# Kernel tuning notes

Hardware: AMD Instinct MI355X
Metric: run time of the kernel (lower is better)

The kernel has to match this reference:

```python
import jax, jax.numpy as jnp
import numpy as np

EPS = 1e-12  # torch F.normalize eps

def _l2norm(v, axis):
    n = jnp.sqrt(jnp.sum(v * v, axis=axis, keepdims=True))
    return v / jnp.maximum(n, EPS)

def setup_inputs() -> dict:
    key = jax.random.key(0)
    k1, k2, k3 = jax.random.split(key, 3)
    N, D, H, W, K = 32, 512, 56, 56, 64
    x = jax.random.normal(k1, (N, D, H, W), dtype=jnp.float32)
    conv_w = jax.random.normal(k2, (K, D), dtype=jnp.float32) * 0.05
    centroids = jax.random.uniform(k3, (K, D), dtype=jnp.float32)
    return {"x": x, "conv_w": conv_w, "centroids": centroids}

def reference(x, conv_w, centroids):
    N, D, H, W = x.shape
    K = centroids.shape[0]
    # descriptor-wise L2 normalization over channel dim
    x = _l2norm(x, axis=1)
    x_flat = x.reshape(N, D, H * W)                      # (N, D, P)
    # 1x1 conv == per-pixel linear map: (K,D) x (N,D,P) -> (N,K,P)
    logits = jnp.einsum('kd,ndp->nkp', conv_w, x_flat)
    soft_assign = jax.nn.softmax(logits, axis=1)         # softmax over clusters
    # vlad[n,k,:] = sum_p a[n,k,p] * (x[n,:,p] - c[k,:])
    #            = (a @ x^T)[n,k,:] - (sum_p a[n,k,p]) * c[k,:]
    agg = jnp.einsum('nkp,ndp->nkd', soft_assign, x_flat)           # (N, K, D)
    a_sum = jnp.sum(soft_assign, axis=2)                            # (N, K)
    vlad = agg - a_sum[:, :, None] * centroids[None, :, :]
    vlad = _l2norm(vlad, axis=2)        # intra-normalization per cluster
    vlad = vlad.reshape(N, K * D)
    vlad = _l2norm(vlad, axis=1)        # global L2 normalization
    return vlad
```

## Files before the change

### kernel.cpp

```cpp
#include <hip/hip_runtime.h>
#include <hip/hip_bf16.h>

typedef unsigned short u16;
typedef unsigned int u32;
typedef __bf16 bf16x8 __attribute__((ext_vector_type(8)));
typedef float f32x4 __attribute__((ext_vector_type(4)));

#define N_ 32
#define D_ 512
#define P_ 3136
#define K_ 64
#define TILES_P 49
#define NDP (D_ * P_)


__device__ __forceinline__ u16 f2bf(float f) {
  u32 u = __float_as_uint(f);
  return (u16)((u + 0x7fffu + ((u >> 16) & 1u)) >> 16);
}
__device__ __forceinline__ u32 pack2(float a, float b) {
  return (u32)f2bf(a) | ((u32)f2bf(b) << 16);
}

__global__ __launch_bounds__(256) void kw_kernel(const float* __restrict__ w,
                                                 u16* __restrict__ wbf) {
  int i = blockIdx.x * 256 + threadIdx.x;
  float4 v = ((const float4*)w)[i];
  ((uint2*)wbf)[i] = make_uint2(pack2(v.x, v.y), pack2(v.z, v.w));
}

__global__ __launch_bounds__(256) void k1_kernel(const float* __restrict__ x,
                                                 const u16* __restrict__ wbf,
                                                 u16* __restrict__ a_ws,
                                                 float* __restrict__ a_sum) {
  __shared__ u16 lds_x[64 * 32];
  __shared__ float a_stage[64][65];
  __shared__ float red[4][64];
  __shared__ float invn_s[64];

  const int t = threadIdx.x;
  const int bid = blockIdx.x;
  const int n = bid / TILES_P;
  const int tile = bid - n * TILES_P;
  const int p0 = tile * 64;
  const int lane = t & 63;
  const int w = t >> 6;
  const int c = lane & 15;
  const int q = lane >> 4;

  const float* xb = x + (size_t)n * NDP + p0 + lane;
  const int wslot = w ^ ((lane >> 1) & 3);
  const int rp = w * 16 + c;
  const int rslot = q ^ ((rp >> 1) & 3);

  f32x4 acc[4];
#pragma unroll
  for (int m = 0; m < 4; ++m) acc[m] = (f32x4){0.f, 0.f, 0.f, 0.f};
  float sumsq = 0.f;

  for (int s = 0; s < 16; ++s) {
    const float* xs = xb + (s * 32 + w * 8) * P_;
    float v[8];
#pragma unroll
    for (int j = 0; j < 8; ++j) v[j] = xs[j * P_];
#pragma unroll
    for (int j = 0; j < 8; ++j) sumsq += v[j] * v[j];
    uint4 pk = make_uint4(pack2(v[0], v[1]), pack2(v[2], v[3]),
                          pack2(v[4], v[5]), pack2(v[6], v[7]));
    __syncthreads();
    ((uint4*)lds_x)[lane * 4 + wslot] = pk;
    __syncthreads();
    bf16x8 bfrag = ((const bf16x8*)lds_x)[rp * 4 + rslot];
#pragma unroll
    for (int m = 0; m < 4; ++m) {
      bf16x8 afrag = ((const bf16x8*)wbf)[(m * 16 + c) * 64 + s * 4 + q];
      acc[m] = __builtin_amdgcn_mfma_f32_16x16x32_bf16(afrag, bfrag, acc[m], 0, 0, 0);
    }
  }

  red[w][lane] = sumsq;
  __syncthreads();
  if (t < 64) {
    float s2 = red[0][t] + red[1][t] + red[2][t] + red[3][t];
    invn_s[t] = 1.f / fmaxf(sqrtf(s2), 1e-12f);
  }
  __syncthreads();

  const float inv_p = invn_s[rp];
  float sc[4][4];
  float lmax = -3.0e38f;
#pragma unroll
  for (int m = 0; m < 4; ++m)
#pragma unroll
    for (int r = 0; r < 4; ++r) {
      float val = acc[m][r] * inv_p;
      sc[m][r] = val;
      lmax = fmaxf(lmax, val);
    }
  lmax = fmaxf(lmax, __shfl_xor(lmax, 16));
  lmax = fmaxf(lmax, __shfl_xor(lmax, 32));
  float lsum = 0.f;
#pragma unroll
  for (int m = 0; m < 4; ++m)
#pragma unroll
    for (int r = 0; r < 4; ++r) {
      float e = __expf(sc[m][r] - lmax);
      sc[m][r] = e;
      lsum += e;
    }
  lsum += __shfl_xor(lsum, 16);
  lsum += __shfl_xor(lsum, 32);
  const float rs = 1.f / lsum;
#pragma unroll
  for (int m = 0; m < 4; ++m)
#pragma unroll
    for (int r = 0; r < 4; ++r)
      a_stage[m * 16 + q * 4 + r][rp] = sc[m][r] * rs;
  __syncthreads();

  {
    const int k = t >> 2, pc = t & 3;
    float ssum = 0.f;
    u32 u[8];
#pragma unroll
    for (int jj = 0; jj < 8; ++jj) {
      int p = pc * 16 + jj * 2;
      float a0 = a_stage[k][p], a1 = a_stage[k][p + 1];
      ssum += a0 + a1;
      u[jj] = (u32)f2bf(a0 * invn_s[p]) | ((u32)f2bf(a1 * invn_s[p + 1]) << 16);
    }
    u16* dst = a_ws + (size_t)n * (K_ * P_) + k * P_ + p0 + pc * 16;
    ((uint4*)dst)[0] = make_uint4(u[0], u[1], u[2], u[3]);
    ((uint4*)dst)[1] = make_uint4(u[4], u[5], u[6], u[7]);
    ssum += __shfl_xor(ssum, 1);
    ssum += __shfl_xor(ssum, 2);
    if ((t & 3) == 0) atomicAdd(&a_sum[n * 64 + k], ssum);
  }
}

__global__ __launch_bounds__(256) void k2_kernel(const float* __restrict__ x,
                                                 const u16* __restrict__ a_ws,
                                                 float* __restrict__ agg) {
  const int bid = blockIdx.x;
  const int n = bid >> 4;
  const int dblk = (bid >> 1) & 7;
  const int pp = bid & 1;
  const int t = threadIdx.x;
  const int lane = t & 63, w = t >> 6;
  const int c = lane & 15, q = lane >> 4;
  const int d0 = dblk * 64 + w * 16;

  f32x4 acc[4];
#pragma unroll
  for (int m = 0; m < 4; ++m) acc[m] = (f32x4){0.f, 0.f, 0.f, 0.f};

  const bf16x8* arow = (const bf16x8*)(a_ws + (size_t)n * (K_ * P_));
  const float4* xf = (const float4*)(x + ((size_t)n * D_ + d0 + c) * P_);
  const int it0 = pp * 49, it1 = it0 + 49;
  for (int it = it0; it < it1; ++it) {
    float4 b0 = xf[it * 8 + q * 2];
    float4 b1 = xf[it * 8 + q * 2 + 1];
    bf16x8 bfrag;
    bfrag[0] = (__bf16)b0.x; bfrag[1] = (__bf16)b0.y;
    bfrag[2] = (__bf16)b0.z; bfrag[3] = (__bf16)b0.w;
    bfrag[4] = (__bf16)b1.x; bfrag[5] = (__bf16)b1.y;
    bfrag[6] = (__bf16)b1.z; bfrag[7] = (__bf16)b1.w;
#pragma unroll
    for (int m = 0; m < 4; ++m) {
      bf16x8 afrag = arow[(m * 16 + c) * 392 + it * 4 + q];
      acc[m] = __builtin_amdgcn_mfma_f32_16x16x32_bf16(afrag, bfrag, acc[m], 0, 0, 0);
    }
  }
  float* ob = agg + ((size_t)pp * 32 + n) * (K_ * D_);
#pragma unroll
  for (int m = 0; m < 4; ++m)
#pragma unroll
    for (int r = 0; r < 4; ++r)
      ob[(m * 16 + q * 4 + r) * D_ + d0 + c] = acc[m][r];
}

__global__ __launch_bounds__(256) void k3_kernel(const float* __restrict__ agg,
                                                 const float* __restrict__ a_sum,
                                                 const float* __restrict__ cent,
                                                 float* __restrict__ out) {
  __shared__ float rowsq[64][4];
  __shared__ float invr[64];
  __shared__ float ginv_s;
  const int n = blockIdx.x;
  const int t = threadIdx.x;
  const int w = t >> 6;
  const float* a0 = agg + (size_t)n * 32768;
  const float* a1 = a0 + 32 * 32768;
  float* o = out + (size_t)n * 32768;
  float s0 = 0.f;
  for (int i = 0; i < 128; ++i) {
    const int e = t + (i << 8);
    const int k = i >> 1;
    float v = a0[e] + a1[e] - a_sum[n * 64 + k] * cent[e];
    o[e] = v;
    float v2 = v * v;
    v2 += __shfl_xor(v2, 1);  v2 += __shfl_xor(v2, 2);  v2 += __shfl_xor(v2, 4);
    v2 += __shfl_xor(v2, 8);  v2 += __shfl_xor(v2, 16); v2 += __shfl_xor(v2, 32);
    if (i & 1) { if ((t & 63) == 0) rowsq[k][w] = s0 + v2; }
    else s0 = v2;
  }
  __syncthreads();
  if (t < 64) {
    float row = rowsq[t][0] + rowsq[t][1] + rowsq[t][2] + rowsq[t][3];
    float ri = 1.f / fmaxf(sqrtf(row), 1e-12f);
    invr[t] = ri;
    float g = row * ri * ri;
    g += __shfl_xor(g, 1); g += __shfl_xor(g, 2); g += __shfl_xor(g, 4);
    g += __shfl_xor(g, 8); g += __shfl_xor(g, 16); g += __shfl_xor(g, 32);
    if (t == 0) ginv_s = 1.f / fmaxf(sqrtf(g), 1e-12f);
  }
  __syncthreads();
  const float gi = ginv_s;
  for (int i = 0; i < 128; ++i) {
    const int e = t + (i << 8);
    o[e] *= invr[i >> 1] * gi;
  }
}

extern "C" void kernel_launch(void* const* d_in, const int* in_sizes, int n_in,
                              void* d_out, int out_size, void* d_ws, size_t ws_size,
                              hipStream_t stream) {
  (void)in_sizes; (void)n_in; (void)out_size; (void)ws_size;
  const float* x    = (const float*)d_in[0];
  const float* cw   = (const float*)d_in[1];
  const float* cent = (const float*)d_in[2];
  float* out = (float*)d_out;
  char* ws = (char*)d_ws;
  u16*   wbf   = (u16*)(ws);
  u16*   a_ws  = (u16*)(ws + 65536);
  float* a_sum = (float*)(ws + 12910592);
  float* agg   = (float*)(ws + 12918784);

  hipMemsetAsync(a_sum, 0, 64 * 32 * sizeof(float), stream);
  kw_kernel<<<32, 256, 0, stream>>>(cw, wbf);
  k1_kernel<<<32 * TILES_P, 256, 0, stream>>>(x, wbf, a_ws, a_sum);
  k2_kernel<<<512, 256, 0, stream>>>(x, a_ws, agg);
  k3_kernel<<<32, 256, 0, stream>>>(agg, a_sum, cent, out);
}
```

Baseline: 454.6 us.

## Drop LDS transpose in k1, split P finer in k2, parallelize finalization

k1 now loads x directly in MFMA B-fragment layout with a register prefetch of the next slice. That removes the LDS staging, both barriers per step and the cross-wave sum-of-squares reduction. k2 splits P into 7 chunks instead of 2, giving 1792 blocks, and double-buffers its global loads. The single 32-block k3 is replaced by a 2048-block partial-sum/residual kernel plus a 256-block scaling kernel. The trade-off is more agg partial traffic (7 copies) and an extra launch.

Result: faster. 393.9 us (-13.3%).

```diff
diff --git a/kernel.cpp b/kernel.cpp
--- a/kernel.cpp
+++ b/kernel.cpp
@@ -33,9 +33,7 @@
                                                  const u16* __restrict__ wbf,
                                                  u16* __restrict__ a_ws,
                                                  float* __restrict__ a_sum) {
-  __shared__ u16 lds_x[64 * 32];
   __shared__ float a_stage[64][65];
-  __shared__ float red[4][64];
   __shared__ float invn_s[64];
 
   const int t = threadIdx.x;
@@ -47,46 +45,48 @@
   const int w = t >> 6;
   const int c = lane & 15;
   const int q = lane >> 4;
-
-  const float* xb = x + (size_t)n * NDP + p0 + lane;
-  const int wslot = w ^ ((lane >> 1) & 3);
   const int rp = w * 16 + c;
-  const int rslot = q ^ ((rp >> 1) & 3);
+
+  const float* xl = x + (size_t)n * NDP + p0 + rp + (size_t)(q * 8) * P_;
 
   f32x4 acc[4];
 #pragma unroll
   for (int m = 0; m < 4; ++m) acc[m] = (f32x4){0.f, 0.f, 0.f, 0.f};
   float sumsq = 0.f;
 
+  float v[8];
+#pragma unroll
+  for (int j = 0; j < 8; ++j) v[j] = xl[j * P_];
+
   for (int s = 0; s < 16; ++s) {
-    const float* xs = xb + (s * 32 + w * 8) * P_;
-    float v[8];
-#pragma unroll
-    for (int j = 0; j < 8; ++j) v[j] = xs[j * P_];
-#pragma unroll
-    for (int j = 0; j < 8; ++j) sumsq += v[j] * v[j];
-    uint4 pk = make_uint4(pack2(v[0], v[1]), pack2(v[2], v[3]),
-                          pack2(v[4], v[5]), pack2(v[6], v[7]));
-    __syncthreads();
-    ((uint4*)lds_x)[lane * 4 + wslot] = pk;
-    __syncthreads();
-    bf16x8 bfrag = ((const bf16x8*)lds_x)[rp * 4 + rslot];
+    float vn[8];
+    if (s < 15) {
+      const float* xs = xl + (size_t)((s + 1) * 32) * P_;
+#pragma unroll
+      for (int j = 0; j < 8; ++j) vn[j] = xs[j * P_];
+    }
+    bf16x8 bfrag;
+#pragma unroll
+    for (int j = 0; j < 8; ++j) {
+      sumsq += v[j] * v[j];
+      bfrag[j] = (__bf16)v[j];
+    }
 #pragma unroll
     for (int m = 0; m < 4; ++m) {
       bf16x8 afrag = ((const bf16x8*)wbf)[(m * 16 + c) * 64 + s * 4 + q];
       acc[m] = __builtin_amdgcn_mfma_f32_16x16x32_bf16(afrag, bfrag, acc[m], 0, 0, 0);
     }
-  }
-
-  red[w][lane] = sumsq;
-  __syncthreads();
-  if (t < 64) {
-    float s2 = red[0][t] + red[1][t] + red[2][t] + red[3][t];
-    invn_s[t] = 1.f / fmaxf(sqrtf(s2), 1e-12f);
-  }
-  __syncthreads();
-
-  const float inv_p = invn_s[rp];
+    if (s < 15) {
+#pragma unroll
+      for (int j = 0; j < 8; ++j) v[j] = vn[j];
+    }
+  }
+
+  sumsq += __shfl_xor(sumsq, 16);
+  sumsq += __shfl_xor(sumsq, 32);
+  const float inv_p = 1.f / fmaxf(sqrtf(sumsq), 1e-12f);
+  if (q == 0) invn_s[rp] = inv_p;
+
   float sc[4][4];
   float lmax = -3.0e38f;
 #pragma unroll
@@ -142,9 +142,10 @@
                                                  const u16* __restrict__ a_ws,
                                                  float* __restrict__ agg) {
   const int bid = blockIdx.x;
-  const int n = bid >> 4;
-  const int dblk = (bid >> 1) & 7;
-  const int pp = bid & 1;
+  const int n = bid / 56;
+  const int rem = bid - n * 56;
+  const int dblk = rem / 7;
+  const int pp = rem - dblk * 7;
   const int t = threadIdx.x;
   const int lane = t & 63, w = t >> 6;
   const int c = lane & 15, q = lane >> 4;
@@ -156,19 +157,38 @@
 
   const bf16x8* arow = (const bf16x8*)(a_ws + (size_t)n * (K_ * P_));
   const float4* xf = (const float4*)(x + ((size_t)n * D_ + d0 + c) * P_);
-  const int it0 = pp * 49, it1 = it0 + 49;
+  const int it0 = pp * 14, it1 = it0 + 14;
+
+  float4 b0 = xf[it0 * 8 + q * 2];
+  float4 b1 = xf[it0 * 8 + q * 2 + 1];
+  bf16x8 af0 = arow[(0 * 16 + c) * 392 + it0 * 4 + q];
+  bf16x8 af1 = arow[(1 * 16 + c) * 392 + it0 * 4 + q];
+  bf16x8 af2 = arow[(2 * 16 + c) * 392 + it0 * 4 + q];
+  bf16x8 af3 = arow[(3 * 16 + c) * 392 + it0 * 4 + q];
+
+#pragma unroll
   for (int it = it0; it < it1; ++it) {
-    float4 b0 = xf[it * 8 + q * 2];
-    float4 b1 = xf[it * 8 + q * 2 + 1];
+    float4 nb0, nb1;
+    bf16x8 nf0, nf1, nf2, nf3;
+    if (it + 1 < it1) {
+      nb0 = xf[(it + 1) * 8 + q * 2];
+      nb1 = xf[(it + 1) * 8 + q * 2 + 1];
+      nf0 = arow[(0 * 16 + c) * 392 + (it + 1) * 4 + q];
+      nf1 = arow[(1 * 16 + c) * 392 + (it + 1) * 4 + q];
+      nf2 = arow[(2 * 16 + c) * 392 + (it + 1) * 4 + q];
+      nf3 = arow[(3 * 16 + c) * 392 + (it + 1) * 4 + q];
+    }
     bf16x8 bfrag;
     bfrag[0] = (__bf16)b0.x; bfrag[1] = (__bf16)b0.y;
     bfrag[2] = (__bf16)b0.z; bfrag[3] = (__bf16)b0.w;
     bfrag[4] = (__bf16)b1.x; bfrag[5] = (__bf16)b1.y;
     bfrag[6] = (__bf16)b1.z; bfrag[7] = (__bf16)b1.w;
-#pragma unroll
-    for (int m = 0; m < 4; ++m) {
-      bf16x8 afrag = arow[(m * 16 + c) * 392 + it * 4 + q];
-      acc[m] = __builtin_amdgcn_mfma_f32_16x16x32_bf16(afrag, bfrag, acc[m], 0, 0, 0);
+    acc[0] = __builtin_amdgcn_mfma_f32_16x16x32_bf16(af0, bfrag, acc[0], 0, 0, 0);
+    acc[1] = __builtin_amdgcn_mfma_f32_16x16x32_bf16(af1, bfrag, acc[1], 0, 0, 0);
+    acc[2] = __builtin_amdgcn_mfma_f32_16x16x32_bf16(af2, bfrag, acc[2], 0, 0, 0);
+    acc[3] = __builtin_amdgcn_mfma_f32_16x16x32_bf16(af3, bfrag, acc[3], 0, 0, 0);
+    if (it + 1 < it1) {
+      b0 = nb0; b1 = nb1; af0 = nf0; af1 = nf1; af2 = nf2; af3 = nf3;
     }
   }
   float* ob = agg + ((size_t)pp * 32 + n) * (K_ * D_);
@@ -179,46 +199,66 @@
       ob[(m * 16 + q * 4 + r) * D_ + d0 + c] = acc[m][r];
 }
 
-__global__ __launch_bounds__(256) void k3_kernel(const float* __restrict__ agg,
+__global__ __launch_bounds__(64) void k3a_kernel(const float* __restrict__ agg,
                                                  const float* __restrict__ a_sum,
                                                  const float* __restrict__ cent,
-                                                 float* __restrict__ out) {
-  __shared__ float rowsq[64][4];
-  __shared__ float invr[64];
-  __shared__ float ginv_s;
-  const int n = blockIdx.x;
-  const int t = threadIdx.x;
-  const int w = t >> 6;
-  const float* a0 = agg + (size_t)n * 32768;
-  const float* a1 = a0 + 32 * 32768;
-  float* o = out + (size_t)n * 32768;
-  float s0 = 0.f;
-  for (int i = 0; i < 128; ++i) {
-    const int e = t + (i << 8);
-    const int k = i >> 1;
-    float v = a0[e] + a1[e] - a_sum[n * 64 + k] * cent[e];
-    o[e] = v;
-    float v2 = v * v;
-    v2 += __shfl_xor(v2, 1);  v2 += __shfl_xor(v2, 2);  v2 += __shfl_xor(v2, 4);
-    v2 += __shfl_xor(v2, 8);  v2 += __shfl_xor(v2, 16); v2 += __shfl_xor(v2, 32);
-    if (i & 1) { if ((t & 63) == 0) rowsq[k][w] = s0 + v2; }
-    else s0 = v2;
-  }
-  __syncthreads();
+                                                 float* __restrict__ out,
+                                                 float* __restrict__ rowsq) {
+  const int b = blockIdx.x;
+  const int n = b >> 6, k = b & 63;
+  const int t = threadIdx.x;
+  const float* ab = agg + ((size_t)n * 64 + k) * 512 + t * 8;
+  float v[8];
+#pragma unroll
+  for (int j = 0; j < 8; ++j) v[j] = 0.f;
+#pragma unroll
+  for (int pp = 0; pp < 7; ++pp) {
+    const float4* p4 = (const float4*)(ab + (size_t)pp * 32 * (K_ * D_));
+    float4 r0 = p4[0], r1 = p4[1];
+    v[0] += r0.x; v[1] += r0.y; v[2] += r0.z; v[3] += r0.w;
+    v[4] += r1.x; v[5] += r1.y; v[6] += r1.z; v[7] += r1.w;
+  }
+  const float asum = a_sum[b];
+  const float4* c4 = (const float4*)(cent + k * 512 + t * 8);
+  float4 c0 = c4[0], c1 = c4[1];
+  v[0] -= asum * c0.x; v[1] -= asum * c0.y; v[2] -= asum * c0.z; v[3] -= asum * c0.w;
+  v[4] -= asum * c1.x; v[5] -= asum * c1.y; v[6] -= asum * c1.z; v[7] -= asum * c1.w;
+  float ss = 0.f;
+#pragma unroll
+  for (int j = 0; j < 8; ++j) ss += v[j] * v[j];
+  ss += __shfl_xor(ss, 1);  ss += __shfl_xor(ss, 2);  ss += __shfl_xor(ss, 4);
+  ss += __shfl_xor(ss, 8);  ss += __shfl_xor(ss, 16); ss += __shfl_xor(ss, 32);
+  float4* o4 = (float4*)(out + (size_t)n * 32768 + k * 512 + t * 8);
+  o4[0] = make_float4(v[0], v[1], v[2], v[3]);
+  o4[1] = make_float4(v[4], v[5], v[6], v[7]);
+  if (t == 0) rowsq[b] = ss;
+}
+
+__global__ __launch_bounds__(256) void k3b_kernel(const float* __restrict__ rowsq,
+                                                  float* __restrict__ out) {
+  __shared__ float invr_s[64];
+  __shared__ float gi_s;
+  const int n = blockIdx.x >> 3;
+  const int seg = blockIdx.x & 7;
+  const int t = threadIdx.x;
   if (t < 64) {
-    float row = rowsq[t][0] + rowsq[t][1] + rowsq[t][2] + rowsq[t][3];
-    float ri = 1.f / fmaxf(sqrtf(row), 1e-12f);
-    invr[t] = ri;
-    float g = row * ri * ri;
+    float r = rowsq[n * 64 + t];
+    float ri = 1.f / fmaxf(sqrtf(r), 1e-12f);
+    invr_s[t] = ri;
+    float g = r * ri * ri;
     g += __shfl_xor(g, 1); g += __shfl_xor(g, 2); g += __shfl_xor(g, 4);
     g += __shfl_xor(g, 8); g += __shfl_xor(g, 16); g += __shfl_xor(g, 32);
-    if (t == 0) ginv_s = 1.f / fmaxf(sqrtf(g), 1e-12f);
+    if (t == 0) gi_s = 1.f / fmaxf(sqrtf(g), 1e-12f);
   }
   __syncthreads();
-  const float gi = ginv_s;
-  for (int i = 0; i < 128; ++i) {
-    const int e = t + (i << 8);
-    o[e] *= invr[i >> 1] * gi;
+  const int e0 = seg * 4096 + t * 16;
+  const float sc = invr_s[e0 >> 9] * gi_s;
+  float4* o4 = (float4*)(out + (size_t)n * 32768 + e0);
+#pragma unroll
+  for (int i = 0; i < 4; ++i) {
+    float4 vv = o4[i];
+    vv.x *= sc; vv.y *= sc; vv.z *= sc; vv.w *= sc;
+    o4[i] = vv;
   }
 }
 
@@ -235,10 +275,12 @@
   u16*   a_ws  = (u16*)(ws + 65536);
   float* a_sum = (float*)(ws + 12910592);
   float* agg   = (float*)(ws + 12918784);
+  float* rowsq = (float*)(ws + 42278912);
 
   hipMemsetAsync(a_sum, 0, 64 * 32 * sizeof(float), stream);
   kw_kernel<<<32, 256, 0, stream>>>(cw, wbf);
   k1_kernel<<<32 * TILES_P, 256, 0, stream>>>(x, wbf, a_ws, a_sum);
-  k2_kernel<<<512, 256, 0, stream>>>(x, a_ws, agg);
-  k3_kernel<<<32, 256, 0, stream>>>(agg, a_sum, cent, out);
-}
+  k2_kernel<<<1792, 256, 0, stream>>>(x, a_ws, agg);
+  k3a_kernel<<<2048, 64, 0, stream>>>(agg, a_sum, cent, out, rowsq);
+  k3b_kernel<<<256, 256, 0, stream>>>(rowsq, out);
+}
```
